# Performance work log

Measured on AMD Instinct MI355X. Metric: run time of the kernel, lower is better.

## Reference

```python
import jax, jax.numpy as jnp
import numpy as np

L_THETAS = (1.0, 0.2, 0.1)
LR = 1.0
C = 10      # num_out_caps
D = 16      # vector_depth
M = 10      # transformation matrices per capsule


def setup_inputs() -> dict:
    key = jax.random.key(0)
    k_in, k_w, k_dc = jax.random.split(key, 3)
    B, H, Wd, F, DIN = 64, 14, 14, 32, 8
    N = H * Wd * F
    inputs = jax.random.normal(k_in, (B, H, Wd, F, DIN), dtype=jnp.float32)
    # glorot-uniform for W: shape [N, input_d, d*m]
    fan_in, fan_out = DIN, D * M
    limit = float(np.sqrt(6.0 / (fan_in + fan_out)))
    W = jax.random.uniform(k_w, (N, DIN, D * M), minval=-limit, maxval=limit, dtype=jnp.float32)
    # digit_caps codebook: RandomUniform(-1, 1), shape [c, d]
    digit_caps = jax.random.uniform(k_dc, (C, D), minval=-1.0, maxval=1.0, dtype=jnp.float32)
    return {"inputs": inputs, "W": W, "digit_caps": digit_caps}


def reference(inputs, W, digit_caps):
    B = inputs.shape[0]
    H, Wd, F, DIN = inputs.shape[1:]
    N = H * Wd * F
    c, d = digit_caps.shape
    m = W.shape[-1] // d

    x = inputs.reshape(B, N, DIN)
    # per-capsule transformation: [B, N, d*m] -> [B, N*m, d]
    u = jnp.einsum('bji,jik->bjk', x, W).reshape(B, N * m, d)
    # squash-like nonlinearity: tanh(|u|)/|u| * u
    n = jnp.linalg.norm(u, axis=-1, keepdims=True)
    u = (jnp.tanh(n) / n) * u

    # Similarities u . digit_caps[c]; the original tiles u over c, but since the
    # winner-take-all mask is constant along d, sum((u*mask_c)*dc) == mask_c * (u.dc).
    sim0 = jnp.einsum('bnd,cd->bnc', u, digit_caps)  # [B, Nm, c]
    mask = jnp.ones_like(sim0)
    accum = jnp.zeros_like(digit_caps)               # sum of sparse updates, reduced over (b, n)
    for theta in L_THETAS:
        sims = sim0 * mask
        winners = jnp.argmax(sims, axis=-1)                        # [B, Nm]
        onehot = jax.nn.one_hot(winners, c, dtype=u.dtype)         # [B, Nm, c]
        # sum_{b,n} onehot * (u - dc) == einsum(onehot, u) - count_c * dc
        accum = accum + (LR * theta) * (
            jnp.einsum('bnc,bnd->cd', onehot, u)
            - jnp.sum(onehot, axis=(0, 1))[:, None] * digit_caps
        )
        mask = mask - onehot

    updates = accum / (B * N * m)   # mean over axes [0, 1] of the [B,Nm,c,d] update tensor
    dc = digit_caps + updates
    dc = dc / jnp.linalg.norm(dc, axis=-1, keepdims=True)

    sim_final = jnp.einsum('bnd,cd->bnc', u, dc)     # [B, Nm, c]
    return jax.nn.softmax(jnp.mean(sim_final, axis=-2), axis=-1)  # [B, c]
```

## Files before the change

kernel.cpp:

```cpp
#include <hip/hip_runtime.h>
#include <hip/hip_fp16.h>
#include <math.h>

#define NPOS 6272
#define DIN_ 8
#define DVEC 16
#define CCAP 10
#define JC 8
#define NBLK (NPOS / JC)
#define PSTRIDE 1200
#define ACC_FLOATS 1194
#define P_OFF 1280
#define SH_WORDS 5760

__device__ __forceinline__ float fdot2u(unsigned a, unsigned b, float c) {
#if __has_builtin(__builtin_amdgcn_fdot2)
    typedef _Float16 h2v __attribute__((ext_vector_type(2)));
    return __builtin_amdgcn_fdot2(__builtin_bit_cast(h2v, a),
                                  __builtin_bit_cast(h2v, b), c, false);
#else
    __half2 p = __hmul2(__builtin_bit_cast(__half2, a), __builtin_bit_cast(__half2, b));
    return c + (__low2float(p) + __high2float(p));
#endif
}
__device__ __forceinline__ unsigned pack_rn(float lo, float hi) {
    return __builtin_bit_cast(unsigned, __floats2half2_rn(lo, hi));
}
__device__ __forceinline__ unsigned umaxu(unsigned a, unsigned b) { return a > b ? a : b; }

__device__ __forceinline__ unsigned qsum_h2(unsigned v) {
    int t = __builtin_amdgcn_mov_dpp((int)v, 0xB1, 0xF, 0xF, true);
    __half2 a = __builtin_bit_cast(__half2, v);
    __half2 b = __builtin_bit_cast(__half2, (unsigned)t);
    a = __hadd2(a, b);
    v = __builtin_bit_cast(unsigned, a);
    t = __builtin_amdgcn_mov_dpp((int)v, 0x4E, 0xF, 0xF, true);
    b = __builtin_bit_cast(__half2, (unsigned)t);
    a = __builtin_bit_cast(__half2, v);
    a = __hadd2(a, b);
    return __builtin_bit_cast(unsigned, a);
}
__device__ __forceinline__ float qsum_f32(float v) {
    int t = __builtin_amdgcn_mov_dpp(__builtin_bit_cast(int, v), 0xB1, 0xF, 0xF, true);
    v += __builtin_bit_cast(float, t);
    t = __builtin_amdgcn_mov_dpp(__builtin_bit_cast(int, v), 0x4E, 0xF, 0xF, true);
    v += __builtin_bit_cast(float, t);
    return v;
}

__device__ __forceinline__ float squash_scale(float nsq) {
    float n = __builtin_amdgcn_sqrtf(nsq);
    float e = __expf(2.0f * n);
    float th = 1.0f - 2.0f * __builtin_amdgcn_rcpf(e + 1.0f);
    return th * __builtin_amdgcn_rcpf(n);
}

__global__ __launch_bounds__(256) void caps_main(
    const float* __restrict__ xin,
    const float* __restrict__ Wg,
    const float* __restrict__ dcg,
    float* __restrict__ P,
    float* __restrict__ ACC)
{
    __shared__ __align__(16) unsigned SH[SH_WORDS];
    __shared__ __align__(16) unsigned dch[84];
    __shared__ __align__(16) unsigned ub_out[4][64][8];

    const int tid  = threadIdx.x;
    const int lane = tid & 63;
    const int wvu  = __builtin_amdgcn_readfirstlane(tid >> 6);
    const int j0   = blockIdx.x * JC;

    for (int g = tid; g < 1280; g += 256) {
        int jk = g / 40, d4 = g - jk * 40;
        int jj = jk >> 2, k = jk & 3;
        const float* s1 = Wg + (size_t)(j0 + jj) * 1280 + (2 * k) * 160 + d4 * 4;
        float4 a = *(const float4*)s1;
        float4 b = *(const float4*)(s1 + 160);
        uint4 w;
        w.x = pack_rn(a.x, b.x); w.y = pack_rn(a.y, b.y);
        w.z = pack_rn(a.z, b.z); w.w = pack_rn(a.w, b.w);
        *(uint4*)(SH + jk * 160 + d4 * 4) = w;
    }
    if (tid < 20) {
        int c = tid >> 1, part = tid & 1;
        const float4* dp = (const float4*)(dcg + c * 16 + part * 8);
        float4 a = dp[0], b = dp[1];
        uint4 w;
        w.x = pack_rn(a.x, a.y); w.y = pack_rn(a.z, a.w);
        w.z = pack_rn(b.x, b.y); w.w = pack_rn(b.z, b.w);
        *(uint4*)(dch + c * 8 + part * 4) = w;
    }

    unsigned xh2[2][4];
    #pragma unroll
    for (int jj2 = 0; jj2 < 2; ++jj2) {
        const float4* xp = (const float4*)(xin + (size_t)lane * (NPOS * DIN_)
                                               + (size_t)(j0 + wvu + 4 * jj2) * DIN_);
        float4 xa = xp[0], xb = xp[1];
        xh2[jj2][0] = pack_rn(xa.x, xa.y); xh2[jj2][1] = pack_rn(xa.z, xa.w);
        xh2[jj2][2] = pack_rn(xb.x, xb.y); xh2[jj2][3] = pack_rn(xb.z, xb.w);
    }
    __syncthreads();

    __half2 S[CCAP][8];
    float   T[CCAP];
    __half2 ub[8];
    #pragma unroll
    for (int c = 0; c < CCAP; ++c) {
        T[c] = 0.0f;
        #pragma unroll
        for (int k = 0; k < 8; ++k) S[c][k] = __float2half2_rn(0.0f);
    }
    #pragma unroll
    for (int k = 0; k < 8; ++k) ub[k] = __float2half2_rn(0.0f);

    const unsigned MASKHI = 0xFFFFFFF0u;

    #pragma unroll 1
    for (int jj2 = 0; jj2 < 2; ++jj2) {
        const unsigned* wbase = SH + (wvu + 4 * jj2) * 640;
        unsigned xh[4];
        #pragma unroll
        for (int k = 0; k < 4; ++k) xh[k] = xh2[jj2][k];

        #pragma unroll 1
        for (int m = 0; m < 10; ++m) {
            float u[DVEC];
            #pragma unroll
            for (int d = 0; d < DVEC; ++d) u[d] = 0.0f;
            #pragma unroll
            for (int k = 0; k < 4; ++k) {
                const uint4* wk = (const uint4*)(wbase + k * 160 + m * 16);
                uint4 q0 = wk[0], q1 = wk[1], q2 = wk[2], q3 = wk[3];
                unsigned xk = xh[k];
                u[0]  = fdot2u(xk, q0.x, u[0]);  u[1]  = fdot2u(xk, q0.y, u[1]);
                u[2]  = fdot2u(xk, q0.z, u[2]);  u[3]  = fdot2u(xk, q0.w, u[3]);
                u[4]  = fdot2u(xk, q1.x, u[4]);  u[5]  = fdot2u(xk, q1.y, u[5]);
                u[6]  = fdot2u(xk, q1.z, u[6]);  u[7]  = fdot2u(xk, q1.w, u[7]);
                u[8]  = fdot2u(xk, q2.x, u[8]);  u[9]  = fdot2u(xk, q2.y, u[9]);
                u[10] = fdot2u(xk, q2.z, u[10]); u[11] = fdot2u(xk, q2.w, u[11]);
                u[12] = fdot2u(xk, q3.x, u[12]); u[13] = fdot2u(xk, q3.y, u[13]);
                u[14] = fdot2u(xk, q3.z, u[14]); u[15] = fdot2u(xk, q3.w, u[15]);
            }

            unsigned uh[8];
            #pragma unroll
            for (int k = 0; k < 8; ++k) uh[k] = pack_rn(u[2 * k], u[2 * k + 1]);

            float sb[CCAP];
            #pragma unroll
            for (int c = 0; c < CCAP; ++c) {
                const uint4* dq = (const uint4*)(dch + c * 8);
                uint4 e0 = dq[0], e1 = dq[1];
                float acc = fdot2u(uh[0], e0.x, 64.0f);
                acc = fdot2u(uh[1], e0.y, acc);
                acc = fdot2u(uh[2], e0.z, acc);
                acc = fdot2u(uh[3], e0.w, acc);
                acc = fdot2u(uh[4], e1.x, acc);
                acc = fdot2u(uh[5], e1.y, acc);
                acc = fdot2u(uh[6], e1.z, acc);
                acc = fdot2u(uh[7], e1.w, acc);
                sb[c] = acc;
            }

            float nsq = fdot2u(uh[0], uh[0], 0.0f);
            nsq = fdot2u(uh[1], uh[1], nsq);
            nsq = fdot2u(uh[2], uh[2], nsq);
            nsq = fdot2u(uh[3], uh[3], nsq);
            float nsqb = fdot2u(uh[4], uh[4], 0.0f);
            nsqb = fdot2u(uh[5], uh[5], nsqb);
            nsqb = fdot2u(uh[6], uh[6], nsqb);
            nsqb = fdot2u(uh[7], uh[7], nsqb);
            float sc = squash_scale(nsq + nsqb);

            unsigned pe[CCAP];
            float w[CCAP];
            #pragma unroll
            for (int c = 0; c < CCAP; ++c)
                pe[c] = (__builtin_bit_cast(unsigned, sb[c]) & MASKHI) | (unsigned)(15 - c);

            unsigned m0 = pe[0];
            #pragma unroll
            for (int c = 1; c < CCAP; ++c) m0 = umaxu(m0, pe[c]);
            #pragma unroll
            for (int c = 0; c < CCAP; ++c) {
                const unsigned zc = 0x42800000u | (unsigned)(15 - c);
                bool e0 = (pe[c] == m0);
                w[c] = e0 ? 1.0f : 0.0f;
                pe[c] = e0 ? zc : pe[c];
            }
            unsigned m1 = pe[0];
            #pragma unroll
            for (int c = 1; c < CCAP; ++c) m1 = umaxu(m1, pe[c]);
            #pragma unroll
            for (int c = 0; c < CCAP; ++c) {
                const unsigned zc = 0x42800000u | (unsigned)(15 - c);
                unsigned ne = (__builtin_bit_cast(unsigned, 128.0f - sb[c]) & MASKHI)
                              | (unsigned)(15 - c);
                bool e1 = (pe[c] == m1);
                w[c] += e1 ? 0.2f : 0.0f;
                unsigned fresh = (m1 == zc) ? ne : zc;
                pe[c] = e1 ? fresh : pe[c];
            }
            unsigned m2 = pe[0];
            #pragma unroll
            for (int c = 1; c < CCAP; ++c) m2 = umaxu(m2, pe[c]);
            #pragma unroll
            for (int c = 0; c < CCAP; ++c) w[c] += (pe[c] == m2) ? 0.1f : 0.0f;

            __half2 sch = __float2half2_rn(sc);
            #pragma unroll
            for (int k = 0; k < 8; ++k)
                ub[k] = __hfma2(sch, __builtin_bit_cast(__half2, uh[k]), ub[k]);

            #pragma unroll
            for (int c = 0; c < CCAP; ++c) {
                T[c] += w[c];
                __half2 wh = __float2half2_rn(w[c] * sc);
                #pragma unroll
                for (int k = 0; k < 8; ++k)
                    S[c][k] = __hfma2(wh, __builtin_bit_cast(__half2, uh[k]), S[c][k]);
            }
        }
    }

    __syncthreads();

    {
        unsigned sq[CCAP][8];
        float tq[CCAP];
        #pragma unroll
        for (int c = 0; c < CCAP; ++c) {
            tq[c] = qsum_f32(T[c]);
            #pragma unroll
            for (int k = 0; k < 8; ++k)
                sq[c][k] = qsum_h2(__builtin_bit_cast(unsigned, S[c][k]));
        }
        if ((lane & 3) == 0) {
            unsigned* row = SH + (wvu * 16 + (lane >> 2)) * 90;
            #pragma unroll
            for (int c = 0; c < CCAP; ++c) {
                #pragma unroll
                for (int k = 0; k < 8; ++k) row[c * 8 + k] = sq[c][k];
                row[80 + c] = __builtin_bit_cast(unsigned, tq[c]);
            }
        }
        #pragma unroll
        for (int k = 0; k < 8; ++k)
            ub_out[wvu][lane][k] = __builtin_bit_cast(unsigned, ub[k]);
    }
    __syncthreads();

    if (P != nullptr) {
        float* prow = P + (size_t)blockIdx.x * PSTRIDE;
        for (int q = tid; q < ACC_FLOATS; q += 256) {
            float v = 0.0f;
            if (q < 160) {
                int wd = (q >> 4) * 8 + ((q & 15) >> 1);
                int hi = q & 1;
                #pragma unroll 8
                for (int r = 0; r < 64; ++r) {
                    __half2 h = __builtin_bit_cast(__half2, SH[r * 90 + wd]);
                    v += hi ? __high2float(h) : __low2float(h);
                }
            } else if (q < 170) {
                #pragma unroll 8
                for (int r = 0; r < 64; ++r)
                    v += __builtin_bit_cast(float, SH[r * 90 + 80 + (q - 160)]);
            } else {
                int x = q - 170, b = x >> 4, d = x & 15;
                #pragma unroll
                for (int w2 = 0; w2 < 4; ++w2) {
                    __half2 h = __builtin_bit_cast(__half2, ub_out[w2][b][d >> 1]);
                    v += (d & 1) ? __high2float(h) : __low2float(h);
                }
            }
            prow[q] = v;
        }
    } else {
        for (int q = tid; q < ACC_FLOATS; q += 256) {
            float v = 0.0f;
            if (q < 160) {
                int wd = (q >> 4) * 8 + ((q & 15) >> 1);
                int hi = q & 1;
                #pragma unroll 8
                for (int r = 0; r < 64; ++r) {
                    __half2 h = __builtin_bit_cast(__half2, SH[r * 90 + wd]);
                    v += hi ? __high2float(h) : __low2float(h);
                }
            } else if (q < 170) {
                #pragma unroll 8
                for (int r = 0; r < 64; ++r)
                    v += __builtin_bit_cast(float, SH[r * 90 + 80 + (q - 160)]);
            } else {
                int x = q - 170, b = x >> 4, d = x & 15;
                #pragma unroll
                for (int w2 = 0; w2 < 4; ++w2) {
                    __half2 h = __builtin_bit_cast(__half2, ub_out[w2][b][d >> 1]);
                    v += (d & 1) ? __high2float(h) : __low2float(h);
                }
            }
            unsafeAtomicAdd(&ACC[q], v);
        }
    }
}

__global__ __launch_bounds__(256) void caps_reduce(const float* __restrict__ P,
                                                   float* __restrict__ ACC)
{
    const int t = threadIdx.x;
    float acc[5] = {0.f, 0.f, 0.f, 0.f, 0.f};
    const int r0 = blockIdx.x * 16;
    for (int r = 0; r < 16; ++r) {
        const float* row = P + (size_t)(r0 + r) * PSTRIDE;
        #pragma unroll
        for (int s = 0; s < 5; ++s) {
            int col = t + 256 * s;
            float v = (col < ACC_FLOATS) ? row[col] : 0.0f;
            acc[s] += v;
        }
    }
    #pragma unroll
    for (int s = 0; s < 5; ++s) {
        int col = t + 256 * s;
        if (col < ACC_FLOATS) unsafeAtomicAdd(&ACC[col], acc[s]);
    }
}

__global__ __launch_bounds__(256) void caps_final(const float* __restrict__ ACC,
                                                  const float* __restrict__ dcg,
                                                  float* __restrict__ outp)
{
    __shared__ float dcn[160];
    __shared__ float rnm[10];
    __shared__ float lg[640];
    const int t = threadIdx.x;

    if (t < 160) {
        int c = t >> 4;
        float d0 = dcg[t];
        float upd = (ACC[t] - ACC[160 + c] * d0) * (float)(1.0 / 4014080.0);
        dcn[t] = d0 + upd;
    }
    __syncthreads();
    if (t < 10) {
        float s = 0.0f;
        #pragma unroll
        for (int d = 0; d < 16; ++d) s += dcn[t * 16 + d] * dcn[t * 16 + d];
        rnm[t] = 1.0f / sqrtf(s);
    }
    __syncthreads();
    if (t < 160) dcn[t] *= rnm[t >> 4];
    __syncthreads();

    for (int q = t; q < 640; q += 256) {
        int b = q / 10, c = q - 10 * b;
        const float* ubp = &ACC[170 + b * 16];
        float s = 0.0f;
        #pragma unroll
        for (int d = 0; d < 16; ++d) s += ubp[d] * dcn[c * 16 + d];
        lg[q] = s * (float)(1.0 / 62720.0);
    }
    __syncthreads();
    if (t < 64) {
        float mx = lg[t * 10];
        #pragma unroll
        for (int c = 1; c < 10; ++c) mx = fmaxf(mx, lg[t * 10 + c]);
        float e[10];
        float ssum = 0.0f;
        #pragma unroll
        for (int c = 0; c < 10; ++c) { e[c] = expf(lg[t * 10 + c] - mx); ssum += e[c]; }
        float inv = 1.0f / ssum;
        #pragma unroll
        for (int c = 0; c < 10; ++c) outp[t * 10 + c] = e[c] * inv;
    }
}

extern "C" void kernel_launch(void* const* d_in, const int* in_sizes, int n_in,
                              void* d_out, int out_size, void* d_ws, size_t ws_size,
                              hipStream_t stream)
{
    const float* xin = (const float*)d_in[0];
    const float* Wg  = (const float*)d_in[1];
    const float* dcg = (const float*)d_in[2];
    float* outp = (float*)d_out;
    float* ws = (float*)d_ws;
    float* ACC = ws;

    const size_t need = (size_t)(P_OFF + (size_t)NBLK * PSTRIDE) * sizeof(float);
    float* P = (ws_size >= need) ? (ws + P_OFF) : nullptr;

    hipMemsetAsync(ACC, 0, ACC_FLOATS * sizeof(float), stream);
    caps_main<<<dim3(NBLK), dim3(256), 0, stream>>>(xin, Wg, dcg, P, ACC);
    if (P) caps_reduce<<<dim3(49), dim3(256), 0, stream>>>(P, ACC);
    caps_final<<<dim3(1), dim3(256), 0, stream>>>(ACC, dcg, outp);
}
```

Before: 110.9 us.

## Halve per-block capsule count and replace atomic reduction with two-stage store reduction

Each block now handles 4 input capsules instead of 8, doubling the grid to 1568 blocks and removing the inner per-capsule loop, which gives more parallelism and less shared-memory weight staging per block. The partial-sum reduction no longer uses a memset plus atomics: a store-based kernel writes 98 partial rows, and a 512-thread final kernel sums them into shared memory before the squash/softmax tail. This removes the memset launch and atomic contention, but doubles the number of per-block partial rows written and read.

Measured after the change: 112.4 us. No clear change (+1.3%).

```diff
diff --git a/kernel.cpp b/kernel.cpp
--- a/kernel.cpp
+++ b/kernel.cpp
@@ -6,11 +6,13 @@
 #define DIN_ 8
 #define DVEC 16
 #define CCAP 10
-#define JC 8
+#define JC 4
 #define NBLK (NPOS / JC)
 #define PSTRIDE 1200
 #define ACC_FLOATS 1194
 #define P_OFF 1280
+#define R_OFF (P_OFF + NBLK * PSTRIDE)
+#define NRED 98
 #define SH_WORDS 5760
 
 __device__ __forceinline__ float fdot2u(unsigned a, unsigned b, float c) {
@@ -70,8 +72,9 @@
     const int lane = tid & 63;
     const int wvu  = __builtin_amdgcn_readfirstlane(tid >> 6);
     const int j0   = blockIdx.x * JC;
-
-    for (int g = tid; g < 1280; g += 256) {
+    const int j    = j0 + wvu;
+
+    for (int g = tid; g < 640; g += 256) {
         int jk = g / 40, d4 = g - jk * 40;
         int jj = jk >> 2, k = jk & 3;
         const float* s1 = Wg + (size_t)(j0 + jj) * 1280 + (2 * k) * 160 + d4 * 4;
@@ -92,14 +95,13 @@
         *(uint4*)(dch + c * 8 + part * 4) = w;
     }
 
-    unsigned xh2[2][4];
-    #pragma unroll
-    for (int jj2 = 0; jj2 < 2; ++jj2) {
+    unsigned xh[4];
+    {
         const float4* xp = (const float4*)(xin + (size_t)lane * (NPOS * DIN_)
-                                               + (size_t)(j0 + wvu + 4 * jj2) * DIN_);
+                                               + (size_t)j * DIN_);
         float4 xa = xp[0], xb = xp[1];
-        xh2[jj2][0] = pack_rn(xa.x, xa.y); xh2[jj2][1] = pack_rn(xa.z, xa.w);
-        xh2[jj2][2] = pack_rn(xb.x, xb.y); xh2[jj2][3] = pack_rn(xb.z, xb.w);
+        xh[0] = pack_rn(xa.x, xa.y); xh[1] = pack_rn(xa.z, xa.w);
+        xh[2] = pack_rn(xb.x, xb.y); xh[3] = pack_rn(xb.z, xb.w);
     }
     __syncthreads();
 
@@ -115,113 +117,106 @@
     #pragma unroll
     for (int k = 0; k < 8; ++k) ub[k] = __float2half2_rn(0.0f);
 
+    const unsigned* wbase = SH + wvu * 640;
     const unsigned MASKHI = 0xFFFFFFF0u;
 
     #pragma unroll 1
-    for (int jj2 = 0; jj2 < 2; ++jj2) {
-        const unsigned* wbase = SH + (wvu + 4 * jj2) * 640;
-        unsigned xh[4];
-        #pragma unroll
-        for (int k = 0; k < 4; ++k) xh[k] = xh2[jj2][k];
-
-        #pragma unroll 1
-        for (int m = 0; m < 10; ++m) {
-            float u[DVEC];
-            #pragma unroll
-            for (int d = 0; d < DVEC; ++d) u[d] = 0.0f;
-            #pragma unroll
-            for (int k = 0; k < 4; ++k) {
-                const uint4* wk = (const uint4*)(wbase + k * 160 + m * 16);
-                uint4 q0 = wk[0], q1 = wk[1], q2 = wk[2], q3 = wk[3];
-                unsigned xk = xh[k];
-                u[0]  = fdot2u(xk, q0.x, u[0]);  u[1]  = fdot2u(xk, q0.y, u[1]);
-                u[2]  = fdot2u(xk, q0.z, u[2]);  u[3]  = fdot2u(xk, q0.w, u[3]);
-                u[4]  = fdot2u(xk, q1.x, u[4]);  u[5]  = fdot2u(xk, q1.y, u[5]);
-                u[6]  = fdot2u(xk, q1.z, u[6]);  u[7]  = fdot2u(xk, q1.w, u[7]);
-                u[8]  = fdot2u(xk, q2.x, u[8]);  u[9]  = fdot2u(xk, q2.y, u[9]);
-                u[10] = fdot2u(xk, q2.z, u[10]); u[11] = fdot2u(xk, q2.w, u[11]);
-                u[12] = fdot2u(xk, q3.x, u[12]); u[13] = fdot2u(xk, q3.y, u[13]);
-                u[14] = fdot2u(xk, q3.z, u[14]); u[15] = fdot2u(xk, q3.w, u[15]);
-            }
-
-            unsigned uh[8];
-            #pragma unroll
-            for (int k = 0; k < 8; ++k) uh[k] = pack_rn(u[2 * k], u[2 * k + 1]);
-
-            float sb[CCAP];
-            #pragma unroll
-            for (int c = 0; c < CCAP; ++c) {
-                const uint4* dq = (const uint4*)(dch + c * 8);
-                uint4 e0 = dq[0], e1 = dq[1];
-                float acc = fdot2u(uh[0], e0.x, 64.0f);
-                acc = fdot2u(uh[1], e0.y, acc);
-                acc = fdot2u(uh[2], e0.z, acc);
-                acc = fdot2u(uh[3], e0.w, acc);
-                acc = fdot2u(uh[4], e1.x, acc);
-                acc = fdot2u(uh[5], e1.y, acc);
-                acc = fdot2u(uh[6], e1.z, acc);
-                acc = fdot2u(uh[7], e1.w, acc);
-                sb[c] = acc;
-            }
-
-            float nsq = fdot2u(uh[0], uh[0], 0.0f);
-            nsq = fdot2u(uh[1], uh[1], nsq);
-            nsq = fdot2u(uh[2], uh[2], nsq);
-            nsq = fdot2u(uh[3], uh[3], nsq);
-            float nsqb = fdot2u(uh[4], uh[4], 0.0f);
-            nsqb = fdot2u(uh[5], uh[5], nsqb);
-            nsqb = fdot2u(uh[6], uh[6], nsqb);
-            nsqb = fdot2u(uh[7], uh[7], nsqb);
-            float sc = squash_scale(nsq + nsqb);
-
-            unsigned pe[CCAP];
-            float w[CCAP];
-            #pragma unroll
-            for (int c = 0; c < CCAP; ++c)
-                pe[c] = (__builtin_bit_cast(unsigned, sb[c]) & MASKHI) | (unsigned)(15 - c);
-
-            unsigned m0 = pe[0];
-            #pragma unroll
-            for (int c = 1; c < CCAP; ++c) m0 = umaxu(m0, pe[c]);
-            #pragma unroll
-            for (int c = 0; c < CCAP; ++c) {
-                const unsigned zc = 0x42800000u | (unsigned)(15 - c);
-                bool e0 = (pe[c] == m0);
-                w[c] = e0 ? 1.0f : 0.0f;
-                pe[c] = e0 ? zc : pe[c];
-            }
-            unsigned m1 = pe[0];
-            #pragma unroll
-            for (int c = 1; c < CCAP; ++c) m1 = umaxu(m1, pe[c]);
-            #pragma unroll
-            for (int c = 0; c < CCAP; ++c) {
-                const unsigned zc = 0x42800000u | (unsigned)(15 - c);
-                unsigned ne = (__builtin_bit_cast(unsigned, 128.0f - sb[c]) & MASKHI)
-                              | (unsigned)(15 - c);
-                bool e1 = (pe[c] == m1);
-                w[c] += e1 ? 0.2f : 0.0f;
-                unsigned fresh = (m1 == zc) ? ne : zc;
-                pe[c] = e1 ? fresh : pe[c];
-            }
-            unsigned m2 = pe[0];
-            #pragma unroll
-            for (int c = 1; c < CCAP; ++c) m2 = umaxu(m2, pe[c]);
-            #pragma unroll
-            for (int c = 0; c < CCAP; ++c) w[c] += (pe[c] == m2) ? 0.1f : 0.0f;
-
-            __half2 sch = __float2half2_rn(sc);
+    for (int m = 0; m < 10; ++m) {
+        float u[DVEC];
+        #pragma unroll
+        for (int d = 0; d < DVEC; ++d) u[d] = 0.0f;
+        #pragma unroll
+        for (int k = 0; k < 4; ++k) {
+            const uint4* wk = (const uint4*)(wbase + k * 160 + m * 16);
+            uint4 q0 = wk[0], q1 = wk[1], q2 = wk[2], q3 = wk[3];
+            unsigned xk = xh[k];
+            u[0]  = fdot2u(xk, q0.x, u[0]);  u[1]  = fdot2u(xk, q0.y, u[1]);
+            u[2]  = fdot2u(xk, q0.z, u[2]);  u[3]  = fdot2u(xk, q0.w, u[3]);
+            u[4]  = fdot2u(xk, q1.x, u[4]);  u[5]  = fdot2u(xk, q1.y, u[5]);
+            u[6]  = fdot2u(xk, q1.z, u[6]);  u[7]  = fdot2u(xk, q1.w, u[7]);
+            u[8]  = fdot2u(xk, q2.x, u[8]);  u[9]  = fdot2u(xk, q2.y, u[9]);
+            u[10] = fdot2u(xk, q2.z, u[10]); u[11] = fdot2u(xk, q2.w, u[11]);
+            u[12] = fdot2u(xk, q3.x, u[12]); u[13] = fdot2u(xk, q3.y, u[13]);
+            u[14] = fdot2u(xk, q3.z, u[14]); u[15] = fdot2u(xk, q3.w, u[15]);
+        }
+
+        unsigned uh[8];
+        #pragma unroll
+        for (int k = 0; k < 8; ++k) uh[k] = pack_rn(u[2 * k], u[2 * k + 1]);
+
+        float sb[CCAP];
+        #pragma unroll
+        for (int c = 0; c < CCAP; ++c) {
+            const uint4* dq = (const uint4*)(dch + c * 8);
+            uint4 e0 = dq[0], e1 = dq[1];
+            float acc = fdot2u(uh[0], e0.x, 64.0f);
+            acc = fdot2u(uh[1], e0.y, acc);
+            acc = fdot2u(uh[2], e0.z, acc);
+            acc = fdot2u(uh[3], e0.w, acc);
+            acc = fdot2u(uh[4], e1.x, acc);
+            acc = fdot2u(uh[5], e1.y, acc);
+            acc = fdot2u(uh[6], e1.z, acc);
+            acc = fdot2u(uh[7], e1.w, acc);
+            sb[c] = acc;
+        }
+
+        float nsq = fdot2u(uh[0], uh[0], 0.0f);
+        nsq = fdot2u(uh[1], uh[1], nsq);
+        nsq = fdot2u(uh[2], uh[2], nsq);
+        nsq = fdot2u(uh[3], uh[3], nsq);
+        float nsqb = fdot2u(uh[4], uh[4], 0.0f);
+        nsqb = fdot2u(uh[5], uh[5], nsqb);
+        nsqb = fdot2u(uh[6], uh[6], nsqb);
+        nsqb = fdot2u(uh[7], uh[7], nsqb);
+        float sc = squash_scale(nsq + nsqb);
+
+        unsigned pe[CCAP];
+        float w[CCAP];
+        #pragma unroll
+        for (int c = 0; c < CCAP; ++c)
+            pe[c] = (__builtin_bit_cast(unsigned, sb[c]) & MASKHI) | (unsigned)(15 - c);
+
+        unsigned m0 = pe[0];
+        #pragma unroll
+        for (int c = 1; c < CCAP; ++c) m0 = umaxu(m0, pe[c]);
+        #pragma unroll
+        for (int c = 0; c < CCAP; ++c) {
+            const unsigned zc = 0x42800000u | (unsigned)(15 - c);
+            bool e0 = (pe[c] == m0);
+            w[c] = e0 ? 1.0f : 0.0f;
+            pe[c] = e0 ? zc : pe[c];
+        }
+        unsigned m1 = pe[0];
+        #pragma unroll
+        for (int c = 1; c < CCAP; ++c) m1 = umaxu(m1, pe[c]);
+        #pragma unroll
+        for (int c = 0; c < CCAP; ++c) {
+            const unsigned zc = 0x42800000u | (unsigned)(15 - c);
+            unsigned ne = (__builtin_bit_cast(unsigned, 128.0f - sb[c]) & MASKHI)
+                          | (unsigned)(15 - c);
+            bool e1 = (pe[c] == m1);
+            w[c] += e1 ? 0.2f : 0.0f;
+            unsigned fresh = (m1 == zc) ? ne : zc;
+            pe[c] = e1 ? fresh : pe[c];
+        }
+        unsigned m2 = pe[0];
+        #pragma unroll
+        for (int c = 1; c < CCAP; ++c) m2 = umaxu(m2, pe[c]);
+        #pragma unroll
+        for (int c = 0; c < CCAP; ++c) w[c] += (pe[c] == m2) ? 0.1f : 0.0f;
+
+        __half2 sch = __float2half2_rn(sc);
+        #pragma unroll
+        for (int k = 0; k < 8; ++k)
+            ub[k] = __hfma2(sch, __builtin_bit_cast(__half2, uh[k]), ub[k]);
+
+        #pragma unroll
+        for (int c = 0; c < CCAP; ++c) {
+            T[c] += w[c];
+            __half2 wh = __float2half2_rn(w[c] * sc);
             #pragma unroll
             for (int k = 0; k < 8; ++k)
-                ub[k] = __hfma2(sch, __builtin_bit_cast(__half2, uh[k]), ub[k]);
-
-            #pragma unroll
-            for (int c = 0; c < CCAP; ++c) {
-                T[c] += w[c];
-                __half2 wh = __float2half2_rn(w[c] * sc);
-                #pragma unroll
-                for (int k = 0; k < 8; ++k)
-                    S[c][k] = __hfma2(wh, __builtin_bit_cast(__half2, uh[k]), S[c][k]);
-            }
+                S[c][k] = __hfma2(wh, __builtin_bit_cast(__half2, uh[k]), S[c][k]);
         }
     }
 
@@ -306,8 +301,8 @@
     }
 }
 
-__global__ __launch_bounds__(256) void caps_reduce(const float* __restrict__ P,
-                                                   float* __restrict__ ACC)
+__global__ __launch_bounds__(256) void caps_reduce_store(const float* __restrict__ P,
+                                                         float* __restrict__ R)
 {
     const int t = threadIdx.x;
     float acc[5] = {0.f, 0.f, 0.f, 0.f, 0.f};
@@ -317,8 +312,29 @@
         #pragma unroll
         for (int s = 0; s < 5; ++s) {
             int col = t + 256 * s;
-            float v = (col < ACC_FLOATS) ? row[col] : 0.0f;
-            acc[s] += v;
+            acc[s] += (col < ACC_FLOATS) ? row[col] : 0.0f;
+        }
+    }
+    float* out = R + (size_t)blockIdx.x * PSTRIDE;
+    #pragma unroll
+    for (int s = 0; s < 5; ++s) {
+        int col = t + 256 * s;
+        if (col < ACC_FLOATS) out[col] = acc[s];
+    }
+}
+
+__global__ __launch_bounds__(256) void caps_reduce(const float* __restrict__ P,
+                                                   float* __restrict__ ACC)
+{
+    const int t = threadIdx.x;
+    float acc[5] = {0.f, 0.f, 0.f, 0.f, 0.f};
+    const int r0 = blockIdx.x * 16;
+    for (int r = 0; r < 16; ++r) {
+        const float* row = P + (size_t)(r0 + r) * PSTRIDE;
+        #pragma unroll
+        for (int s = 0; s < 5; ++s) {
+            int col = t + 256 * s;
+            acc[s] += (col < ACC_FLOATS) ? row[col] : 0.0f;
         }
     }
     #pragma unroll
@@ -328,53 +344,81 @@
     }
 }
 
-__global__ __launch_bounds__(256) void caps_final(const float* __restrict__ ACC,
-                                                  const float* __restrict__ dcg,
-                                                  float* __restrict__ outp)
-{
+__device__ __forceinline__ void final_core(const float* A, const float* dcg,
+                                           float* outp, int t, int nthr,
+                                           float* dcn, float* rnm, float* lg)
+{
+    if (t < 160) {
+        int c = t >> 4;
+        float d0 = dcg[t];
+        float upd = (A[t] - A[160 + c] * d0) * (float)(1.0 / 4014080.0);
+        dcn[t] = d0 + upd;
+    }
+    __syncthreads();
+    if (t < 10) {
+        float s = 0.0f;
+        #pragma unroll
+        for (int d = 0; d < 16; ++d) s += dcn[t * 16 + d] * dcn[t * 16 + d];
+        rnm[t] = 1.0f / sqrtf(s);
+    }
+    __syncthreads();
+    if (t < 160) dcn[t] *= rnm[t >> 4];
+    __syncthreads();
+
+    for (int q = t; q < 640; q += nthr) {
+        int b = q / 10, c = q - 10 * b;
+        const float* ubp = &A[170 + b * 16];
+        float s = 0.0f;
+        #pragma unroll
+        for (int d = 0; d < 16; ++d) s += ubp[d] * dcn[c * 16 + d];
+        lg[q] = s * (float)(1.0 / 62720.0);
+    }
+    __syncthreads();
+    if (t < 64) {
+        float mx = lg[t * 10];
+        #pragma unroll
+        for (int c = 1; c < 10; ++c) mx = fmaxf(mx, lg[t * 10 + c]);
+        float e[10];
+        float ssum = 0.0f;
+        #pragma unroll
+        for (int c = 0; c < 10; ++c) { e[c] = expf(lg[t * 10 + c] - mx); ssum += e[c]; }
+        float inv = 1.0f / ssum;
+        #pragma unroll
+        for (int c = 0; c < 10; ++c) outp[t * 10 + c] = e[c] * inv;
+    }
+}
+
+__global__ __launch_bounds__(512) void caps_final2(const float* __restrict__ R,
+                                                   const float* __restrict__ dcg,
+                                                   float* __restrict__ outp)
+{
+    __shared__ float A[ACC_FLOATS];
     __shared__ float dcn[160];
     __shared__ float rnm[10];
     __shared__ float lg[640];
     const int t = threadIdx.x;
-
-    if (t < 160) {
-        int c = t >> 4;
-        float d0 = dcg[t];
-        float upd = (ACC[t] - ACC[160 + c] * d0) * (float)(1.0 / 4014080.0);
-        dcn[t] = d0 + upd;
-    }
-    __syncthreads();
-    if (t < 10) {
-        float s = 0.0f;
-        #pragma unroll
-        for (int d = 0; d < 16; ++d) s += dcn[t * 16 + d] * dcn[t * 16 + d];
-        rnm[t] = 1.0f / sqrtf(s);
-    }
-    __syncthreads();
-    if (t < 160) dcn[t] *= rnm[t >> 4];
-    __syncthreads();
-
-    for (int q = t; q < 640; q += 256) {
-        int b = q / 10, c = q - 10 * b;
-        const float* ubp = &ACC[170 + b * 16];
-        float s = 0.0f;
-        #pragma unroll
-        for (int d = 0; d < 16; ++d) s += ubp[d] * dcn[c * 16 + d];
-        lg[q] = s * (float)(1.0 / 62720.0);
-    }
-    __syncthreads();
-    if (t < 64) {
-        float mx = lg[t * 10];
-        #pragma unroll
-        for (int c = 1; c < 10; ++c) mx = fmaxf(mx, lg[t * 10 + c]);
-        float e[10];
-        float ssum = 0.0f;
-        #pragma unroll
-        for (int c = 0; c < 10; ++c) { e[c] = expf(lg[t * 10 + c] - mx); ssum += e[c]; }
-        float inv = 1.0f / ssum;
-        #pragma unroll
-        for (int c = 0; c < 10; ++c) outp[t * 10 + c] = e[c] * inv;
-    }
+    for (int q = t; q < ACC_FLOATS; q += 512) {
+        float v = 0.0f;
+        #pragma unroll 7
+        for (int r = 0; r < NRED; ++r) v += R[(size_t)r * PSTRIDE + q];
+        A[q] = v;
+    }
+    __syncthreads();
+    final_core(A, dcg, outp, t, 512, dcn, rnm, lg);
+}
+
+__global__ __launch_bounds__(256) void caps_final(const float* __restrict__ ACC,
+                                                  const float* __restrict__ dcg,
+                                                  float* __restrict__ outp)
+{
+    __shared__ float dcn[160];
+    __shared__ float rnm[10];
+    __shared__ float lg[640];
+    __shared__ float A[ACC_FLOATS];
+    const int t = threadIdx.x;
+    for (int q = t; q < ACC_FLOATS; q += 256) A[q] = ACC[q];
+    __syncthreads();
+    final_core(A, dcg, outp, t, 256, dcn, rnm, lg);
 }
 
 extern "C" void kernel_launch(void* const* d_in, const int* in_sizes, int n_in,
@@ -388,11 +432,24 @@
     float* ws = (float*)d_ws;
     float* ACC = ws;
 
-    const size_t need = (size_t)(P_OFF + (size_t)NBLK * PSTRIDE) * sizeof(float);
-    float* P = (ws_size >= need) ? (ws + P_OFF) : nullptr;
-
-    hipMemsetAsync(ACC, 0, ACC_FLOATS * sizeof(float), stream);
-    caps_main<<<dim3(NBLK), dim3(256), 0, stream>>>(xin, Wg, dcg, P, ACC);
-    if (P) caps_reduce<<<dim3(49), dim3(256), 0, stream>>>(P, ACC);
-    caps_final<<<dim3(1), dim3(256), 0, stream>>>(ACC, dcg, outp);
-}
+    const size_t needA = (size_t)(R_OFF + (size_t)NRED * PSTRIDE) * sizeof(float);
+    const size_t needB = (size_t)(P_OFF + (size_t)NBLK * PSTRIDE) * sizeof(float);
+
+    if (ws_size >= needA) {
+        float* P = ws + P_OFF;
+        float* R = ws + R_OFF;
+        caps_main<<<dim3(NBLK), dim3(256), 0, stream>>>(xin, Wg, dcg, P, ACC);
+        caps_reduce_store<<<dim3(NRED), dim3(256), 0, stream>>>(P, R);
+        caps_final2<<<dim3(1), dim3(512), 0, stream>>>(R, dcg, outp);
+    } else if (ws_size >= needB) {
+        float* P = ws + P_OFF;
+        hipMemsetAsync(ACC, 0, ACC_FLOATS * sizeof(float), stream);
+        caps_main<<<dim3(NBLK), dim3(256), 0, stream>>>(xin, Wg, dcg, P, ACC);
+        caps_reduce<<<dim3(NRED), dim3(256), 0, stream>>>(P, ACC);
+        caps_final<<<dim3(1), dim3(256), 0, stream>>>(ACC, dcg, outp);
+    } else {
+        hipMemsetAsync(ACC, 0, ACC_FLOATS * sizeof(float), stream);
+        caps_main<<<dim3(NBLK), dim3(256), 0, stream>>>(xin, Wg, dcg, nullptr, ACC);
+        caps_final<<<dim3(1), dim3(256), 0, stream>>>(ACC, dcg, outp);
+    }
+}
```
